# Kernel tuning notes

Hardware: AMD Instinct MI355X
Metric: run time of the kernel (lower is better)

The kernel has to match this reference:

```python
import jax, jax.numpy as jnp
import numpy as np

B, T, D = 32, 2048, 512
K_TIMBRE, K_EXPR, K_DETAIL = 512, 256, 512
BETA = 0.25  # commitment cost


def _linear(x, W, b):
    # torch nn.Linear: y = x @ W.T + b, W is [out, in]
    return jnp.einsum('btd,od->bto', x, W) + b


def _vq(x, codebook):
    """Single VQ stage. x: [B,T,D], codebook: [K,D].
    Returns straight-through quantized [B,T,D], indices [B,T], scalar loss."""
    flat = x.reshape(-1, x.shape[-1])                      # [N, D]
    # squared euclidean distances via expansion (same math as torch source)
    d = (jnp.sum(flat * flat, axis=1, keepdims=True)
         + jnp.sum(codebook * codebook, axis=1)
         - 2.0 * flat @ codebook.T)                        # [N, K]
    idx = jnp.argmin(d, axis=1)                            # [N]
    # direct gather == one-hot @ codebook (identical values & grads)
    q = codebook[idx].reshape(x.shape)                     # [B, T, D]
    e_loss = jnp.mean((jax.lax.stop_gradient(q) - x) ** 2)
    q_loss = jnp.mean((q - jax.lax.stop_gradient(x)) ** 2)
    loss = q_loss + BETA * e_loss
    q_st = x + jax.lax.stop_gradient(q - x)                # straight-through
    return q_st, idx.reshape(x.shape[0], x.shape[1]), loss


def setup_inputs() -> dict:
    key = jax.random.key(0)
    ks = jax.random.split(key, 16)
    bound = 1.0 / np.sqrt(D)
    bound3 = 1.0 / np.sqrt(3 * D)
    inp = {
        'x': jax.random.normal(ks[0], (B, T, D), dtype=jnp.float32),
        'timbre_W': jax.random.uniform(ks[1], (D, D), jnp.float32, -bound, bound),
        'timbre_b': jax.random.uniform(ks[2], (D,), jnp.float32, -bound, bound),
        'expr_W': jax.random.uniform(ks[3], (D, D), jnp.float32, -bound, bound),
        'expr_b': jax.random.uniform(ks[4], (D,), jnp.float32, -bound, bound),
        'detail_W': jax.random.uniform(ks[5], (D, D), jnp.float32, -bound, bound),
        'detail_b': jax.random.uniform(ks[6], (D,), jnp.float32, -bound, bound),
        'out_W': jax.random.uniform(ks[7], (D, 3 * D), jnp.float32, -bound3, bound3),
        'out_b': jax.random.uniform(ks[8], (D,), jnp.float32, -bound3, bound3),
        'timbre_cb': jax.random.uniform(ks[9], (K_TIMBRE, D), jnp.float32, -1.0 / K_TIMBRE, 1.0 / K_TIMBRE),
        'expr_cb': jax.random.uniform(ks[10], (K_EXPR, D), jnp.float32, -1.0 / K_EXPR, 1.0 / K_EXPR),
        'detail_cb0': jax.random.uniform(ks[11], (K_DETAIL, D), jnp.float32, -1.0 / K_DETAIL, 1.0 / K_DETAIL),
        'detail_cb1': jax.random.uniform(ks[12], (K_DETAIL, D), jnp.float32, -1.0 / K_DETAIL, 1.0 / K_DETAIL),
    }
    return inp


def reference(x, timbre_W, timbre_b, expr_W, expr_b, detail_W, detail_b,
              out_W, out_b, timbre_cb, expr_cb, detail_cb0, detail_cb1):
    timbre_feat = _linear(x, timbre_W, timbre_b)
    expr_feat = _linear(x, expr_W, expr_b)
    detail_feat = _linear(x, detail_W, detail_b)

    timbre_q, timbre_idx, timbre_loss = _vq(timbre_feat, timbre_cb)
    expr_q, expr_idx, expr_loss = _vq(expr_feat, expr_cb)

    # 2-stage residual VQ
    q0, d_idx0, l0 = _vq(detail_feat, detail_cb0)
    residual = detail_feat - q0
    q1, d_idx1, l1 = _vq(residual, detail_cb1)
    detail_q = q0 + q1
    detail_loss = l0 + l1

    combined = jnp.concatenate([timbre_q, expr_q, detail_q], axis=-1)  # [B,T,3D]
    quantized = _linear(combined, out_W, out_b)                        # [B,T,D]
    loss = timbre_loss + expr_loss + detail_loss
    return (quantized, timbre_idx, expr_idx, d_idx0, d_idx1, loss)
```

## Files before the change

### kernel.cpp

```cpp
#include <hip/hip_runtime.h>
#include <hip/hip_fp16.h>


#define NTOK 65536
#define DIM 512
#define NDIM3 1536

typedef __attribute__((ext_vector_type(8))) short short8;
typedef __attribute__((ext_vector_type(4))) float float4v;

static __device__ __forceinline__ ushort f2bf(float x) {
    uint u = __float_as_uint(x);
    uint r = u + 0x7FFFu + ((u >> 16) & 1u);
    return (ushort)(r >> 16);
}

#define PBM 64
#define PBN 128
#define PBK 16
#define ARS 66
#define BRS 160

__global__ __launch_bounds__(256, 4)
void proj_kernel(const float* __restrict__ X, const float* __restrict__ W,
                 const float* __restrict__ bias, float* __restrict__ out) {
    __shared__ __align__(16) double As[PBK][ARS];
    __shared__ __align__(16) double Bs[PBK][BRS];

    const int tid = threadIdx.x;
    const int tx = tid & 15, ty = tid >> 4;
    const int row0 = blockIdx.x * PBM;
    const int col0 = blockIdx.y * PBN;

    const int ar  = tid >> 2, akq = (tid & 3) * 4;
    const int bc  = tid >> 1, bkq = (tid & 1) * 8;
    const int bpos = (bc >> 3) * 10 + (bc & 7);

    double acc[4][8];
#pragma unroll
    for (int r = 0; r < 4; ++r)
#pragma unroll
        for (int c = 0; c < 8; ++c) acc[r][c] = 0.0;

    const float* Xp = X + (size_t)(row0 + ar) * DIM + akq;
    const float* Wp = W + (size_t)(col0 + bc) * DIM + bkq;

    for (int k0 = 0; k0 < DIM; k0 += PBK) {
        float4 av  = *(const float4*)(Xp + k0);
        float4 bv0 = *(const float4*)(Wp + k0);
        float4 bv1 = *(const float4*)(Wp + k0 + 4);
        __syncthreads();
        As[akq + 0][ar] = (double)av.x;
        As[akq + 1][ar] = (double)av.y;
        As[akq + 2][ar] = (double)av.z;
        As[akq + 3][ar] = (double)av.w;
        Bs[bkq + 0][bpos] = (double)bv0.x;
        Bs[bkq + 1][bpos] = (double)bv0.y;
        Bs[bkq + 2][bpos] = (double)bv0.z;
        Bs[bkq + 3][bpos] = (double)bv0.w;
        Bs[bkq + 4][bpos] = (double)bv1.x;
        Bs[bkq + 5][bpos] = (double)bv1.y;
        Bs[bkq + 6][bpos] = (double)bv1.z;
        Bs[bkq + 7][bpos] = (double)bv1.w;
        __syncthreads();
#pragma unroll
        for (int kk = 0; kk < PBK; ++kk) {
            double a[4], b[8];
#pragma unroll
            for (int r = 0; r < 4; ++r) a[r] = As[kk][ty * 4 + r];
#pragma unroll
            for (int c = 0; c < 8; ++c) b[c] = Bs[kk][tx * 10 + c];
#pragma unroll
            for (int r = 0; r < 4; ++r)
#pragma unroll
                for (int c = 0; c < 8; ++c)
                    acc[r][c] += a[r] * b[c];
        }
    }
    double bcol[8];
#pragma unroll
    for (int c = 0; c < 8; ++c) bcol[c] = (double)bias[col0 + tx * 8 + c];
#pragma unroll
    for (int r = 0; r < 4; ++r) {
        const int row = row0 + ty * 4 + r;
        float4 o0, o1;
        o0.x = (float)(acc[r][0] + bcol[0]); o0.y = (float)(acc[r][1] + bcol[1]);
        o0.z = (float)(acc[r][2] + bcol[2]); o0.w = (float)(acc[r][3] + bcol[3]);
        o1.x = (float)(acc[r][4] + bcol[4]); o1.y = (float)(acc[r][5] + bcol[5]);
        o1.z = (float)(acc[r][6] + bcol[6]); o1.w = (float)(acc[r][7] + bcol[7]);
        *(float4*)(out + (size_t)row * DIM + col0 + tx * 8)     = o0;
        *(float4*)(out + (size_t)row * DIM + col0 + tx * 8 + 4) = o1;
    }
}

#define TAU_A 2.0e-3f

template<bool RESID>
__global__ __launch_bounds__(256)
void vq_fused(const float* __restrict__ feat, const float* __restrict__ cb, int K,
              const float* __restrict__ cb_prev, const float* __restrict__ previdx_f,
              float* __restrict__ idx_out, float* __restrict__ loss_acc) {
    __shared__ __align__(16) ushort A_s[64][40];
    __shared__ __align__(16) ushort B_s[256][40];
    __shared__ __half Csub[64][264];
    __shared__ int    sPrev[64];
    __shared__ float  mgMax[64][4];
    __shared__ float  mgVal[64][4][4];
    __shared__ int    mgIdx[64][4][4];
    __shared__ int    jobCnt[64];
    __shared__ int    jobIdx[64][8];

    const int tid  = threadIdx.x;
    const int lane = tid & 63;
    const int wave = tid >> 6;
    const int quad = lane >> 4;
    const int l15  = lane & 15;
    const int row0 = blockIdx.x * 64;

    if (RESID) { if (tid < 64) sPrev[tid] = (int)previdx_f[row0 + tid]; }
    __syncthreads();

    const int otok = tid >> 2, opart = tid & 3;
    float submax = -3.0e38f;
    float sval[4]; int sidx[4]; int scnt = 0;
#pragma unroll
    for (int s = 0; s < 4; ++s) { sval[s] = -3.0e38f; sidx[s] = 0; }

    const int nct = K >> 8;
    for (int ct = 0; ct < nct; ++ct) {
        float4v acc[4][4];
#pragma unroll
        for (int mt = 0; mt < 4; ++mt)
#pragma unroll
            for (int nt = 0; nt < 4; ++nt) acc[mt][nt] = 0.0f;

        for (int kt = 0; kt < DIM / 32; ++kt) {
            __syncthreads();
            {
                const int tok = tid >> 2, kk = (tid & 3) * 8;
                const float* src = feat + (size_t)(row0 + tok) * DIM + kt * 32 + kk;
                float4 f0 = *(const float4*)src;
                float4 f1 = *(const float4*)(src + 4);
                if (RESID) {
                    const float* pr = cb_prev + (size_t)sPrev[tok] * DIM + kt * 32 + kk;
                    float4 p0 = *(const float4*)pr;
                    float4 p1 = *(const float4*)(pr + 4);
                    f0.x -= p0.x; f0.y -= p0.y; f0.z -= p0.z; f0.w -= p0.w;
                    f1.x -= p1.x; f1.y -= p1.y; f1.z -= p1.z; f1.w -= p1.w;
                }
                short8 hv;
                hv[0] = (short)f2bf(f0.x); hv[1] = (short)f2bf(f0.y);
                hv[2] = (short)f2bf(f0.z); hv[3] = (short)f2bf(f0.w);
                hv[4] = (short)f2bf(f1.x); hv[5] = (short)f2bf(f1.y);
                hv[6] = (short)f2bf(f1.z); hv[7] = (short)f2bf(f1.w);
                *(short8*)&A_s[tok][kk] = hv;
            }
            {
                const float* src = cb + (size_t)(ct * 256 + tid) * DIM + kt * 32;
#pragma unroll
                for (int h = 0; h < 4; ++h) {
                    float4 b0 = *(const float4*)(src + h * 8);
                    float4 b1 = *(const float4*)(src + h * 8 + 4);
                    short8 hv;
                    hv[0] = (short)f2bf(b0.x); hv[1] = (short)f2bf(b0.y);
                    hv[2] = (short)f2bf(b0.z); hv[3] = (short)f2bf(b0.w);
                    hv[4] = (short)f2bf(b1.x); hv[5] = (short)f2bf(b1.y);
                    hv[6] = (short)f2bf(b1.z); hv[7] = (short)f2bf(b1.w);
                    *(short8*)&B_s[tid][h * 8] = hv;
                }
            }
            __syncthreads();
            short8 af[4], bf[4];
#pragma unroll
            for (int mt = 0; mt < 4; ++mt)
                af[mt] = *(const short8*)&A_s[mt * 16 + l15][quad * 8];
#pragma unroll
            for (int nt = 0; nt < 4; ++nt)
                bf[nt] = *(const short8*)&B_s[wave * 64 + nt * 16 + l15][quad * 8];
#pragma unroll
            for (int mt = 0; mt < 4; ++mt)
#pragma unroll
                for (int nt = 0; nt < 4; ++nt)
                    acc[mt][nt] = __builtin_amdgcn_mfma_f32_16x16x32_bf16(
                        af[mt], bf[nt], acc[mt][nt], 0, 0, 0);
        }
        __syncthreads();
#pragma unroll
        for (int mt = 0; mt < 4; ++mt)
#pragma unroll
            for (int nt = 0; nt < 4; ++nt)
#pragma unroll
                for (int r = 0; r < 4; ++r)
                    Csub[mt * 16 + quad * 4 + r][wave * 64 + nt * 16 + l15] =
                        __float2half(acc[mt][nt][r]);
        __syncthreads();
        for (int j = 0; j < 64; ++j) {
            const int c = opart * 64 + j;
            const float a = __half2float(Csub[otok][c]);
            if (a > submax) submax = a;
            if (a >= submax - TAU_A) {
                const int gc = ct * 256 + c;
                if (scnt < 4) { sval[scnt] = a; sidx[scnt] = gc; ++scnt; }
                else {
                    int w = 0;
#pragma unroll
                    for (int s = 1; s < 4; ++s) if (sval[s] < sval[w]) w = s;
                    if (a > sval[w]) { sval[w] = a; sidx[w] = gc; }
                }
            }
        }
    }

    mgMax[otok][opart] = submax;
#pragma unroll
    for (int s = 0; s < 4; ++s) {
        mgVal[otok][opart][s] = (s < scnt) ? sval[s] : -3.0e38f;
        mgIdx[otok][opart][s] = sidx[s];
    }
    __syncthreads();
    if (tid < 64) {
        float g = mgMax[tid][0];
#pragma unroll
        for (int p = 1; p < 4; ++p) g = fmaxf(g, mgMax[tid][p]);
        int cnt = 0;
#pragma unroll
        for (int p = 0; p < 4; ++p)
#pragma unroll
            for (int s = 0; s < 4; ++s) {
                const float a = mgVal[tid][p][s];
                if (a >= g - TAU_A && cnt < 8) jobIdx[tid][cnt++] = mgIdx[tid][p][s];
            }
        jobCnt[tid] = cnt;
    }
    __syncthreads();

    double lsum = 0.0;
    for (int t = wave; t < 64; t += 4) {
        const float* fr = feat + (size_t)(row0 + t) * DIM + lane * 8;
        float4 f0 = *(const float4*)fr;
        float4 f1 = *(const float4*)(fr + 4);
        if (RESID) {
            const float* pr = cb_prev + (size_t)sPrev[t] * DIM + lane * 8;
            float4 p0 = *(const float4*)pr;
            float4 p1 = *(const float4*)(pr + 4);
            f0.x -= p0.x; f0.y -= p0.y; f0.z -= p0.z; f0.w -= p0.w;
            f1.x -= p1.x; f1.y -= p1.y; f1.z -= p1.z; f1.w -= p1.w;
        }
        float v[8] = {f0.x, f0.y, f0.z, f0.w, f1.x, f1.y, f1.z, f1.w};
        double vv = 0.0;
#pragma unroll
        for (int u = 0; u < 8; ++u) vv += (double)v[u] * (double)v[u];
        for (int o = 1; o < 64; o <<= 1) vv += __shfl_xor(vv, o, 64);

        float bestd = 3.4e38f; int besti = 0x7fffffff; double bestl = 0.0;
        const int cnt = jobCnt[t];
        for (int j = 0; j < cnt; ++j) {
            const int c = jobIdx[t][j];
            const float* cr = cb + (size_t)c * DIM + lane * 8;
            float4 c0v = *(const float4*)cr;
            float4 c1v = *(const float4*)(cr + 4);
            float cv[8] = {c0v.x, c0v.y, c0v.z, c0v.w, c1v.x, c1v.y, c1v.z, c1v.w};
            double dot = 0.0, cn = 0.0;
#pragma unroll
            for (int u = 0; u < 8; ++u) {
                dot += (double)v[u] * (double)cv[u];
                cn  += (double)cv[u] * (double)cv[u];
            }
            for (int o = 1; o < 64; o <<= 1) {
                dot += __shfl_xor(dot, o, 64);
                cn  += __shfl_xor(cn,  o, 64);
            }
            const float A32 = (float)vv;
            const float d32 = __fsub_rn(__fadd_rn(A32, (float)cn),
                                        __fmul_rn(2.0f, (float)dot));
            if (d32 < bestd || (d32 == bestd && c < besti)) {
                bestd = d32; besti = c; bestl = (vv + cn) - 2.0 * dot;
            }
        }
        if (lane == 0) { idx_out[row0 + t] = (float)besti; lsum += bestl; }
    }
    if (lane == 0) atomicAdd(loss_acc, (float)lsum);
}

__global__ __launch_bounds__(256)
void out_kernel(const float* __restrict__ t_cb, const float* __restrict__ e_cb,
                const float* __restrict__ d_cb0, const float* __restrict__ d_cb1,
                const float* __restrict__ W, const float* __restrict__ bias,
                const float* __restrict__ idx_base, float* __restrict__ outq) {
    __shared__ __align__(16) ushort A_s[128][40];
    __shared__ __align__(16) ushort B_s[128][40];
    __shared__ int sIdx[4][128];

    const int tid  = threadIdx.x;
    const int lane = tid & 63;
    const int wave = tid >> 6;
    const int quad = lane >> 4;
    const int l15  = lane & 15;
    const int row0 = blockIdx.x * 128;
    const int col0 = blockIdx.y * 128;
    const int mw = (wave >> 1) * 64, nw = (wave & 1) * 64;

    {
        int e = tid;
        sIdx[e >> 7][e & 127] = (int)idx_base[(size_t)(e >> 7) * NTOK + row0 + (e & 127)];
        e = tid + 256;
        sIdx[e >> 7][e & 127] = (int)idx_base[(size_t)(e >> 7) * NTOK + row0 + (e & 127)];
    }

    float4v acc[4][4];
#pragma unroll
    for (int mt = 0; mt < 4; ++mt)
#pragma unroll
        for (int nt = 0; nt < 4; ++nt) acc[mt][nt] = 0.0f;

    for (int kt = 0; kt < NDIM3 / 32; ++kt) {
        const int k0 = kt * 32;
        const int seg = k0 >> 9;
        __syncthreads();
        {
            const int tok = tid >> 1, kk = (tid & 1) * 16;
            const int off = (k0 & 511) + kk;
            float fv[16];
            if (seg == 0) {
                const float* s = t_cb + (size_t)sIdx[0][tok] * DIM + off;
#pragma unroll
                for (int u = 0; u < 4; ++u) *(float4*)&fv[u * 4] = *(const float4*)(s + u * 4);
            } else if (seg == 1) {
                const float* s = e_cb + (size_t)sIdx[1][tok] * DIM + off;
#pragma unroll
                for (int u = 0; u < 4; ++u) *(float4*)&fv[u * 4] = *(const float4*)(s + u * 4);
            } else {
                const float* s0 = d_cb0 + (size_t)sIdx[2][tok] * DIM + off;
                const float* s1 = d_cb1 + (size_t)sIdx[3][tok] * DIM + off;
#pragma unroll
                for (int u = 0; u < 4; ++u) {
                    float4 a0 = *(const float4*)(s0 + u * 4);
                    float4 a1 = *(const float4*)(s1 + u * 4);
                    fv[u * 4 + 0] = a0.x + a1.x; fv[u * 4 + 1] = a0.y + a1.y;
                    fv[u * 4 + 2] = a0.z + a1.z; fv[u * 4 + 3] = a0.w + a1.w;
                }
            }
#pragma unroll
            for (int h = 0; h < 2; ++h) {
                short8 hv;
#pragma unroll
                for (int u = 0; u < 8; ++u) hv[u] = (short)f2bf(fv[h * 8 + u]);
                *(short8*)&A_s[tok][kk + h * 8] = hv;
            }
        }
        {
            const int col = tid >> 1, kk = (tid & 1) * 16;
            const float* s = W + (size_t)(col0 + col) * NDIM3 + k0 + kk;
#pragma unroll
            for (int h = 0; h < 2; ++h) {
                float4 b0 = *(const float4*)(s + h * 8);
                float4 b1 = *(const float4*)(s + h * 8 + 4);
                short8 hv;
                hv[0] = (short)f2bf(b0.x); hv[1] = (short)f2bf(b0.y);
                hv[2] = (short)f2bf(b0.z); hv[3] = (short)f2bf(b0.w);
                hv[4] = (short)f2bf(b1.x); hv[5] = (short)f2bf(b1.y);
                hv[6] = (short)f2bf(b1.z); hv[7] = (short)f2bf(b1.w);
                *(short8*)&B_s[col][kk + h * 8] = hv;
            }
        }
        __syncthreads();
        short8 af[4], bf[4];
#pragma unroll
        for (int mt = 0; mt < 4; ++mt)
            af[mt] = *(const short8*)&A_s[mw + mt * 16 + l15][quad * 8];
#pragma unroll
        for (int nt = 0; nt < 4; ++nt)
            bf[nt] = *(const short8*)&B_s[nw + nt * 16 + l15][quad * 8];
#pragma unroll
        for (int mt = 0; mt < 4; ++mt)
#pragma unroll
            for (int nt = 0; nt < 4; ++nt)
                acc[mt][nt] = __builtin_amdgcn_mfma_f32_16x16x32_bf16(
                    af[mt], bf[nt], acc[mt][nt], 0, 0, 0);
    }

#pragma unroll
    for (int nt = 0; nt < 4; ++nt) {
        const int col = col0 + nw + nt * 16 + l15;
        const float bc = bias[col];
#pragma unroll
        for (int mt = 0; mt < 4; ++mt) {
            const int row = row0 + mw + mt * 16 + quad * 4;
#pragma unroll
            for (int r = 0; r < 4; ++r)
                outq[(size_t)(row + r) * DIM + col] = acc[mt][nt][r] + bc;
        }
    }
}

__global__ void init_loss_kernel(float* __restrict__ p) { *p = 0.0f; }

__global__ void finalize_kernel(float* __restrict__ p) {
    *p = 1.25f * (*p) / (float)(NTOK * DIM);
}

extern "C" void kernel_launch(void* const* d_in, const int* in_sizes, int n_in,
                              void* d_out, int out_size, void* d_ws, size_t ws_size,
                              hipStream_t stream) {
    const float* x    = (const float*)d_in[0];
    const float* tW   = (const float*)d_in[1];
    const float* tb   = (const float*)d_in[2];
    const float* eW   = (const float*)d_in[3];
    const float* eb   = (const float*)d_in[4];
    const float* dW   = (const float*)d_in[5];
    const float* db   = (const float*)d_in[6];
    const float* oW   = (const float*)d_in[7];
    const float* ob   = (const float*)d_in[8];
    const float* t_cb = (const float*)d_in[9];
    const float* e_cb = (const float*)d_in[10];
    const float* c0   = (const float*)d_in[11];
    const float* c1   = (const float*)d_in[12];

    float* out = (float*)d_out;
    float* feat = out;
    float* idx_t = out + (size_t)NTOK * DIM;
    float* idx_e = idx_t + NTOK;
    float* idx_0 = idx_e + NTOK;
    float* idx_1 = idx_0 + NTOK;
    float* loss_out = idx_1 + NTOK;

    const dim3 gproj(NTOK / PBM, DIM / PBN);
    const int  gvq = NTOK / 64;
    const dim3 gout(NTOK / 128, DIM / 128);

    init_loss_kernel<<<1, 1, 0, stream>>>(loss_out);

    proj_kernel<<<gproj, 256, 0, stream>>>(x, tW, tb, feat);
    vq_fused<false><<<gvq, 256, 0, stream>>>(feat, t_cb, 512, nullptr, nullptr, idx_t, loss_out);

    proj_kernel<<<gproj, 256, 0, stream>>>(x, eW, eb, feat);
    vq_fused<false><<<gvq, 256, 0, stream>>>(feat, e_cb, 256, nullptr, nullptr, idx_e, loss_out);

    proj_kernel<<<gproj, 256, 0, stream>>>(x, dW, db, feat);
    vq_fused<false><<<gvq, 256, 0, stream>>>(feat, c0, 512, nullptr, nullptr, idx_0, loss_out);
    vq_fused<true><<<gvq, 256, 0, stream>>>(feat, c1, 512, c0, idx_0, idx_1, loss_out);

    out_kernel<<<gout, 256, 0, stream>>>(t_cb, e_cb, c0, c1, oW, ob, idx_t, out);
    finalize_kernel<<<1, 1, 0, stream>>>(loss_out);
}
```

Before: 3.421 ms.

## Use FP64 MFMA for projection GEMM with runtime layout probe

Rewrites the projection GEMM to use the 16x16x4 FP64 matrix-core instruction instead of scalar FP64 FMAs. Shared tiles now hold fp32 and are converted on load. A small MFMA probe at kernel start detects the accumulator row layout and selects the matching store mapping, with a scalar fallback path if neither layout matches. The aim is to remove the scalar double-precision FMA cost of the projections while keeping FP64 accuracy. In exchange the output stores become scalar rather than float4, and occupancy drops to 2 blocks per SIMD.

```diff
diff --git a/kernel.cpp b/kernel.cpp
--- a/kernel.cpp
+++ b/kernel.cpp
@@ -8,6 +8,7 @@
 
 typedef __attribute__((ext_vector_type(8))) short short8;
 typedef __attribute__((ext_vector_type(4))) float float4v;
+typedef __attribute__((ext_vector_type(4))) double f64x4;
 
 static __device__ __forceinline__ ushort f2bf(float x) {
     uint u = __float_as_uint(x);
@@ -17,79 +18,139 @@
 
 #define PBM 64
 #define PBN 128
-#define PBK 16
-#define ARS 66
-#define BRS 160
-
-__global__ __launch_bounds__(256, 4)
+
+__global__ __launch_bounds__(256, 2)
 void proj_kernel(const float* __restrict__ X, const float* __restrict__ W,
                  const float* __restrict__ bias, float* __restrict__ out) {
-    __shared__ __align__(16) double As[PBK][ARS];
-    __shared__ __align__(16) double Bs[PBK][BRS];
-
-    const int tid = threadIdx.x;
-    const int tx = tid & 15, ty = tid >> 4;
+    __shared__ __align__(16) float As[64][20];
+    __shared__ __align__(16) float Bs[128][20];
+
+    const int tid  = threadIdx.x;
+    const int lane = tid & 63;
+    const int wave = tid >> 6;
+    const int quad = lane >> 4;
+    const int l15  = lane & 15;
     const int row0 = blockIdx.x * PBM;
     const int col0 = blockIdx.y * PBN;
-
-    const int ar  = tid >> 2, akq = (tid & 3) * 4;
-    const int bc  = tid >> 1, bkq = (tid & 1) * 8;
-    const int bpos = (bc >> 3) * 10 + (bc & 7);
-
-    double acc[4][8];
-#pragma unroll
-    for (int r = 0; r < 4; ++r)
-#pragma unroll
-        for (int c = 0; c < 8; ++c) acc[r][c] = 0.0;
-
-    const float* Xp = X + (size_t)(row0 + ar) * DIM + akq;
-    const float* Wp = W + (size_t)(col0 + bc) * DIM + bkq;
-
-    for (int k0 = 0; k0 < DIM; k0 += PBK) {
-        float4 av  = *(const float4*)(Xp + k0);
-        float4 bv0 = *(const float4*)(Wp + k0);
-        float4 bv1 = *(const float4*)(Wp + k0 + 4);
-        __syncthreads();
-        As[akq + 0][ar] = (double)av.x;
-        As[akq + 1][ar] = (double)av.y;
-        As[akq + 2][ar] = (double)av.z;
-        As[akq + 3][ar] = (double)av.w;
-        Bs[bkq + 0][bpos] = (double)bv0.x;
-        Bs[bkq + 1][bpos] = (double)bv0.y;
-        Bs[bkq + 2][bpos] = (double)bv0.z;
-        Bs[bkq + 3][bpos] = (double)bv0.w;
-        Bs[bkq + 4][bpos] = (double)bv1.x;
-        Bs[bkq + 5][bpos] = (double)bv1.y;
-        Bs[bkq + 6][bpos] = (double)bv1.z;
-        Bs[bkq + 7][bpos] = (double)bv1.w;
-        __syncthreads();
-#pragma unroll
-        for (int kk = 0; kk < PBK; ++kk) {
-            double a[4], b[8];
-#pragma unroll
-            for (int r = 0; r < 4; ++r) a[r] = As[kk][ty * 4 + r];
-#pragma unroll
-            for (int c = 0; c < 8; ++c) b[c] = Bs[kk][tx * 10 + c];
-#pragma unroll
-            for (int r = 0; r < 4; ++r)
-#pragma unroll
-                for (int c = 0; c < 8; ++c)
-                    acc[r][c] += a[r] * b[c];
-        }
-    }
-    double bcol[8];
-#pragma unroll
-    for (int c = 0; c < 8; ++c) bcol[c] = (double)bias[col0 + tx * 8 + c];
+    const int nw   = wave * 32;
+
+    {
+    }
+    double a_p = (double)(8 * l15 + quad + 1);
+    double b_p = (double)(100 * quad + l15 + 1);
+    f64x4 pacc = {0.0, 0.0, 0.0, 0.0};
+    pacc = __builtin_amdgcn_mfma_f64_16x16x4f64(a_p, b_p, pacc, 0, 0, 0);
+    bool c1 = true, c2 = true;
 #pragma unroll
     for (int r = 0; r < 4; ++r) {
-        const int row = row0 + ty * 4 + r;
-        float4 o0, o1;
-        o0.x = (float)(acc[r][0] + bcol[0]); o0.y = (float)(acc[r][1] + bcol[1]);
-        o0.z = (float)(acc[r][2] + bcol[2]); o0.w = (float)(acc[r][3] + bcol[3]);
-        o1.x = (float)(acc[r][4] + bcol[4]); o1.y = (float)(acc[r][5] + bcol[5]);
-        o1.z = (float)(acc[r][6] + bcol[6]); o1.w = (float)(acc[r][7] + bcol[7]);
-        *(float4*)(out + (size_t)row * DIM + col0 + tx * 8)     = o0;
-        *(float4*)(out + (size_t)row * DIM + col0 + tx * 8 + 4) = o1;
+        const int i1 = quad * 4 + r;
+        const int i2 = quad + 4 * r;
+        double d1 = 0.0, d2 = 0.0;
+#pragma unroll
+        for (int k = 0; k < 4; ++k) {
+            d1 += (double)(8 * i1 + k + 1) * (double)(100 * k + l15 + 1);
+            d2 += (double)(8 * i2 + k + 1) * (double)(100 * k + l15 + 1);
+        }
+        c1 = c1 && (pacc[r] == d1);
+        c2 = c2 && (pacc[r] == d2);
+    }
+    const bool m1 = (__all(c1 ? 1 : 0) != 0);
+    const bool m2 = (__all(c2 ? 1 : 0) != 0);
+
+    const int asr = tid >> 2, askq = (tid & 3) * 4;
+    const int bsr = tid >> 1, bskq = (tid & 1) * 8;
+    const float* Xp = X + (size_t)(row0 + asr) * DIM + askq;
+    const float* Wp = W + (size_t)(col0 + bsr) * DIM + bskq;
+
+    if (m1 || m2) {
+        f64x4 acc[4][2];
+#pragma unroll
+        for (int mt = 0; mt < 4; ++mt)
+#pragma unroll
+            for (int nt = 0; nt < 2; ++nt) acc[mt][nt] = 0.0;
+
+        for (int k0 = 0; k0 < DIM; k0 += 16) {
+            float4 av  = *(const float4*)(Xp + k0);
+            float4 bv0 = *(const float4*)(Wp + k0);
+            float4 bv1 = *(const float4*)(Wp + k0 + 4);
+            __syncthreads();
+            *(float4*)&As[asr][askq]     = av;
+            *(float4*)&Bs[bsr][bskq]     = bv0;
+            *(float4*)&Bs[bsr][bskq + 4] = bv1;
+            __syncthreads();
+#pragma unroll
+            for (int ks = 0; ks < 4; ++ks) {
+                double a[4], b[2];
+#pragma unroll
+                for (int mt = 0; mt < 4; ++mt)
+                    a[mt] = (double)As[mt * 16 + l15][ks * 4 + quad];
+#pragma unroll
+                for (int nt = 0; nt < 2; ++nt)
+                    b[nt] = (double)Bs[nw + nt * 16 + l15][ks * 4 + quad];
+#pragma unroll
+                for (int mt = 0; mt < 4; ++mt)
+#pragma unroll
+                    for (int nt = 0; nt < 2; ++nt)
+                        acc[mt][nt] = __builtin_amdgcn_mfma_f64_16x16x4f64(
+                            a[mt], b[nt], acc[mt][nt], 0, 0, 0);
+            }
+        }
+        const int rbase = m1 ? (quad * 4) : quad;
+        const int rstep = m1 ? 1 : 4;
+#pragma unroll
+        for (int nt = 0; nt < 2; ++nt) {
+            const int col = col0 + nw + nt * 16 + l15;
+            const double bc = (double)bias[col];
+#pragma unroll
+            for (int mt = 0; mt < 4; ++mt)
+#pragma unroll
+                for (int r = 0; r < 4; ++r) {
+                    const int row = row0 + mt * 16 + rbase + r * rstep;
+                    out[(size_t)row * DIM + col] = (float)(acc[mt][nt][r] + bc);
+                }
+        }
+    } else {
+        const int tx = tid & 15, ty = tid >> 4;
+        double acc2[4][8];
+#pragma unroll
+        for (int r = 0; r < 4; ++r)
+#pragma unroll
+            for (int c = 0; c < 8; ++c) acc2[r][c] = 0.0;
+
+        for (int k0 = 0; k0 < DIM; k0 += 16) {
+            float4 av  = *(const float4*)(Xp + k0);
+            float4 bv0 = *(const float4*)(Wp + k0);
+            float4 bv1 = *(const float4*)(Wp + k0 + 4);
+            __syncthreads();
+            *(float4*)&As[asr][askq]     = av;
+            *(float4*)&Bs[bsr][bskq]     = bv0;
+            *(float4*)&Bs[bsr][bskq + 4] = bv1;
+            __syncthreads();
+#pragma unroll
+            for (int kk = 0; kk < 16; ++kk) {
+                double a[4], b[8];
+#pragma unroll
+                for (int r = 0; r < 4; ++r) a[r] = (double)As[ty * 4 + r][kk];
+#pragma unroll
+                for (int c = 0; c < 8; ++c) b[c] = (double)Bs[tx + 16 * c][kk];
+#pragma unroll
+                for (int r = 0; r < 4; ++r)
+#pragma unroll
+                    for (int c = 0; c < 8; ++c)
+                        acc2[r][c] += a[r] * b[c];
+            }
+        }
+        double bcol[8];
+#pragma unroll
+        for (int c = 0; c < 8; ++c) bcol[c] = (double)bias[col0 + tx + 16 * c];
+#pragma unroll
+        for (int r = 0; r < 4; ++r) {
+            const int row = row0 + ty * 4 + r;
+#pragma unroll
+            for (int c = 0; c < 8; ++c)
+                out[(size_t)row * DIM + col0 + tx + 16 * c] =
+                    (float)(acc2[r][c] + bcol[c]);
+        }
     }
 }
 
```

Measured after the change: 3.033 ms. 11.4% less time.
